# Optimization experiments

Measured on AMD Instinct MI355X. Metric: run time of the kernel, lower is better.

The kernel has to match this reference:

```python
import jax, jax.numpy as jnp
import numpy as np
from jax import lax


def _h0_entropy(img):
    """Persistence entropy of the 0-dim sublevel-set persistence diagram of a 2D
    image, using the vertex-based cubical complex (pixels = vertices, 4-neighbor
    edges with filtration value max(endpoints)). Essential (infinite) class is
    excluded. Computed via Kruskal-style union-find with the elder rule."""
    H, W = img.shape
    N = H * W
    vals = img.reshape(N)
    vals_sg = lax.stop_gradient(vals)  # pairing indices are non-differentiable

    idx = jnp.arange(N, dtype=jnp.int32).reshape(H, W)
    eu = jnp.concatenate([idx[:, :-1].ravel(), idx[:-1, :].ravel()])
    ev = jnp.concatenate([idx[:, 1:].ravel(), idx[1:, :].ravel()])
    E = eu.shape[0]  # H*(W-1) + (H-1)*W

    # process edges in increasing filtration order (sublevel filtration)
    w_sg = jnp.maximum(vals_sg[eu], vals_sg[ev])
    order = jnp.argsort(w_sg)
    eu = eu[order]
    ev = ev[order]

    def find(parent, u):
        return lax.while_loop(lambda x: parent[x] != x, lambda x: parent[x], u)

    def body(i, st):
        parent, rb, ob, odu, odv = st
        u = eu[i]
        v = ev[i]
        ru = find(parent, u)
        rv = find(parent, v)
        # one-shot path compression
        parent = parent.at[u].set(ru).at[v].set(rv)
        bu = rb[ru]  # birth-vertex index of each root's component
        bv = rb[rv]
        u_young = vals_sg[bu] >= vals_sg[bv]  # elder rule: later birth dies
        younger = jnp.where(u_young, ru, rv)
        elder = jnp.where(u_young, rv, ru)
        diff = ru != rv
        ob = ob.at[i].set(jnp.where(diff, rb[younger], -1))
        odu = odu.at[i].set(jnp.where(diff, u, 0))
        odv = odv.at[i].set(jnp.where(diff, v, 0))
        parent = parent.at[younger].set(jnp.where(diff, elder, younger))
        return (parent, rb, ob, odu, odv)

    init = (
        jnp.arange(N, dtype=jnp.int32),          # parent
        jnp.arange(N, dtype=jnp.int32),          # birth vertex per root
        -jnp.ones(E, dtype=jnp.int32),           # birth vertex per pair
        jnp.zeros(E, dtype=jnp.int32),           # death edge endpoint u
        jnp.zeros(E, dtype=jnp.int32),           # death edge endpoint v
    )
    _, _, ob, odu, odv = lax.fori_loop(0, E, body, init)

    valid = ob >= 0
    births = vals[jnp.clip(ob, 0)]
    deaths = jnp.maximum(vals[odu], vals[odv])
    pers = jnp.where(valid, deaths - births, 0.0)
    pers = jnp.maximum(pers, 0.0)
    total = jnp.sum(pers)
    p = pers / jnp.maximum(total, jnp.asarray(1e-12, pers.dtype))
    safe_p = jnp.where(p > 0, p, 1.0)
    return -jnp.sum(jnp.where(p > 0, p * jnp.log(safe_p), 0.0))


def setup_inputs() -> dict:
    key = jax.random.key(0)
    x = jax.random.normal(key, (8, 8, 96, 96), dtype=jnp.float32)
    return {"x": x}


def reference(x):
    B, C, H, W = x.shape
    flat = x.reshape(B * C, H, W)
    ents = jax.vmap(_h0_entropy)(flat)  # [B*C]
    # TopoHead stacks per-channel features along dim=1; maxdim=0 -> one
    # persistence-entropy value per (batch, channel).
    return ents.reshape(B, C, 1)
```

## Files before the change

### kernel.cpp

```cpp
#include <hip/hip_runtime.h>

#define H_ 96
#define W_ 96
#define NV (H_ * W_)
#define NT 1024
#define WELEM 576
#define NSUB 9

#define ARENA_BYTES 136192

__device__ __forceinline__ float keyToFloat(unsigned int k) {
  return __uint_as_float((k & 0x80000000u) ? (k ^ 0x80000000u) : ~k);
}
__device__ __forceinline__ unsigned int bitsToKey(unsigned int b) {
  return b ^ ((b & 0x80000000u) ? 0xFFFFFFFFu : 0x80000000u);
}

__global__ __launch_bounds__(NT, 1)
void topo_pk(const float* __restrict__ x, float* __restrict__ out) {
  __shared__ unsigned int arenaW[ARENA_BYTES / 4];
  __shared__ unsigned int waveS[16];
  __shared__ unsigned int waveB[16];
  __shared__ double Td[16], Sd[16];
  unsigned char* arena = (unsigned char*)arenaW;
  unsigned int*   Ka    = (unsigned int*)(arena);
  unsigned int*   Kb    = (unsigned int*)(arena + 36864);
  unsigned short* Pa    = (unsigned short*)(arena + 73728);
  unsigned short* Pb    = (unsigned short*)(arena + 92160);
  unsigned int*   hist  = (unsigned int*)(arena + 110592);
  unsigned char*  incB  = (unsigned char*)(arena + 126976);
  unsigned short* parU  = (unsigned short*)(arena + 92160);
  unsigned int*   claim = (unsigned int*)(arena + 36864);

  const int tid = threadIdx.x;
  const int wv = tid >> 6, ln = tid & 63;
  const float* img = x + (size_t)blockIdx.x * NV;

  const int wbase = wv * WELEM;
  for (int pass = 0; pass < 4; ++pass) {
    const unsigned int*   Ks = (pass & 1) ? Kb : Ka;
    const unsigned short* Ps = (pass & 1) ? Pb : Pa;
    unsigned int*   Kd = (pass & 1) ? Ka : Kb;
    unsigned short* Pd = (pass & 1) ? Pa : Pb;
    const int sh = pass << 3;

    for (int i = tid; i < 16 * 256; i += NT) hist[i] = 0u;
    __syncthreads();

    unsigned kreg[NSUB];
    unsigned rk[NSUB];
    #pragma unroll
    for (int j = 0; j < NSUB; ++j) {
      const int e = wbase + j * 64 + ln;
      const unsigned k = (pass == 0) ? bitsToKey(__float_as_uint(img[e])) : Ks[e];
      kreg[j] = k;
      const unsigned d = (k >> sh) & 255u;
      unsigned long long mask = ~0ull;
      #pragma unroll
      for (int b = 0; b < 8; ++b) {
        const unsigned long long bb = __ballot((d >> b) & 1u);
        mask &= ((d >> b) & 1u) ? bb : ~bb;
      }
      const unsigned long long below = mask & ((1ull << ln) - 1ull);
      const unsigned old = hist[wv * 256 + d];
      rk[j] = (d << 16) | (old + (unsigned)__popcll(below));
      if (below == 0ull)
        hist[wv * 256 + d] = old + (unsigned)__popcll(mask);
    }
    __syncthreads();

    {
      unsigned v0, v1, v2, v3;
      const int s0 = tid * 4;
      v0 = hist[((s0 + 0) & 15) * 256 + ((s0 + 0) >> 4)];
      v1 = hist[((s0 + 1) & 15) * 256 + ((s0 + 1) >> 4)];
      v2 = hist[((s0 + 2) & 15) * 256 + ((s0 + 2) >> 4)];
      v3 = hist[((s0 + 3) & 15) * 256 + ((s0 + 3) >> 4)];
      const unsigned ts = v0 + v1 + v2 + v3;
      unsigned incl = ts;
      #pragma unroll
      for (int off = 1; off < 64; off <<= 1) {
        const unsigned n = (unsigned)__shfl_up((int)incl, off, 64);
        if (ln >= off) incl += n;
      }
      if (ln == 63) waveS[wv] = incl;
      __syncthreads();
      if (tid < 16) {
        unsigned s = 0;
        for (int q = 0; q < 16; ++q) { if (q == tid) break; s += waveS[q]; }
        waveB[tid] = s;
      }
      __syncthreads();
      unsigned run = waveB[wv] + (incl - ts);
      hist[((s0 + 0) & 15) * 256 + ((s0 + 0) >> 4)] = run; run += v0;
      hist[((s0 + 1) & 15) * 256 + ((s0 + 1) >> 4)] = run; run += v1;
      hist[((s0 + 2) & 15) * 256 + ((s0 + 2) >> 4)] = run; run += v2;
      hist[((s0 + 3) & 15) * 256 + ((s0 + 3) >> 4)] = run;
    }
    __syncthreads();

    #pragma unroll
    for (int j = 0; j < NSUB; ++j) {
      const int e = wbase + j * 64 + ln;
      const unsigned d = rk[j] >> 16;
      const unsigned dest = hist[wv * 256 + d] + (rk[j] & 0xFFFFu);
      Kd[dest] = kreg[j];
      Pd[dest] = (pass == 0) ? (unsigned short)e : Ps[e];
    }
    __syncthreads();
  }

  for (int t = tid; t < NV; t += NT) parU[Pa[t]] = (unsigned short)(0x8000u | (unsigned)t);
  for (int i = tid; i < NV; i += NT) claim[i] = 0xFFFFFFFFu;
  for (int v = tid; v < NV; v += NT) {
    const unsigned kc = bitsToKey(__float_as_uint(img[v]));
    const int r = v / W_, c = v - r * W_;
    unsigned b = 0;
    if (c > 0       && bitsToKey(__float_as_uint(img[v - 1]))  <= kc) b |= 1u;
    if (c < W_ - 1  && bitsToKey(__float_as_uint(img[v + 1]))  <= kc) b |= 2u;
    if (r > 0       && bitsToKey(__float_as_uint(img[v - W_])) <= kc) b |= 4u;
    if (r < H_ - 1  && bitsToKey(__float_as_uint(img[v + W_])) <= kc) b |= 8u;
    incB[v] = (unsigned char)b;
  }
  __syncthreads();

  double T = 0.0, S = 0.0;
  unsigned gr = 0;
  for (int ch = 0; ch < NV / NT; ++ch) {
    const int t = ch * NT + tid;
    const int vid = (int)Pa[t];
    const float vt = keyToFloat(Ka[t]);
    const int nv0 = vid - 1, nv1 = vid + 1, nv2 = vid - W_, nv3 = vid + W_;
    const unsigned ib = incB[vid];
    const bool inc0 = (ib & 1u) != 0u;
    const bool inc1 = (ib & 2u) != 0u;
    const bool inc2 = (ib & 4u) != 0u;
    const bool inc3 = (ib & 8u) != 0u;
    int x0 = inc0 ? nv0 : vid, x1 = inc1 ? nv1 : vid;
    int x2 = inc2 ? nv2 : vid, x3 = inc3 ? nv3 : vid;
    unsigned e0 = 0, e1 = 0, e2 = 0, e3 = 0;
    bool committed = false;

    for (;;) {
      const unsigned cval = ((0x000FFFFFu - gr) << 10) | (unsigned)tid;
      ++gr;
      if (!committed) {
        bool d0 = !inc0, d1 = !inc1, d2 = !inc2, d3 = !inc3;
        while (!(d0 && d1 && d2 && d3)) {
          if (!d0) { unsigned e = parU[x0]; if (e & 0x8000u) { e0 = e; d0 = true; } else x0 = (int)e; }
          if (!d1) { unsigned e = parU[x1]; if (e & 0x8000u) { e1 = e; d1 = true; } else x1 = (int)e; }
          if (!d2) { unsigned e = parU[x2]; if (e & 0x8000u) { e2 = e; d2 = true; } else x2 = (int)e; }
          if (!d3) { unsigned e = parU[x3]; if (e & 0x8000u) { e3 = e; d3 = true; } else x3 = (int)e; }
        }
        if (inc0 && nv0 != x0) parU[nv0] = (unsigned short)x0;
        if (inc1 && nv1 != x1) parU[nv1] = (unsigned short)x1;
        if (inc2 && nv2 != x2) parU[nv2] = (unsigned short)x2;
        if (inc3 && nv3 != x3) parU[nv3] = (unsigned short)x3;
      }
      bool u0 = false, u1 = false, u2 = false, u3 = false, uv = false;
      int mvid = vid;
      int rr0 = 0, rr1 = 0, rr2 = 0, rr3 = 0;
      if (!committed) {
        int mrank = t;
        rr0 = (int)(e0 & 0x3FFFu); rr1 = (int)(e1 & 0x3FFFu);
        rr2 = (int)(e2 & 0x3FFFu); rr3 = (int)(e3 & 0x3FFFu);
        if (inc0 && rr0 < mrank) { mrank = rr0; mvid = x0; }
        if (inc1 && rr1 < mrank) { mrank = rr1; mvid = x1; }
        if (inc2 && rr2 < mrank) { mrank = rr2; mvid = x2; }
        if (inc3 && rr3 < mrank) { mrank = rr3; mvid = x3; }
        u0 = inc0 && (x0 != mvid);
        u1 = inc1 && (x1 != mvid) && !(inc0 && x1 == x0);
        u2 = inc2 && (x2 != mvid) && !(inc0 && x2 == x0) && !(inc1 && x2 == x1);
        u3 = inc3 && (x3 != mvid) && !(inc0 && x3 == x0) && !(inc1 && x3 == x1) && !(inc2 && x3 == x2);
        uv = (mvid != vid);
        if (u0) atomicMin(&claim[x0], cval);
        if (u1) atomicMin(&claim[x1], cval);
        if (u2) atomicMin(&claim[x2], cval);
        if (u3) atomicMin(&claim[x3], cval);
        if (uv) atomicMin(&claim[vid], cval);
      }
      __syncthreads();
      if (!committed) {
        bool win = true;
        if (u0 && claim[x0] != cval) win = false;
        if (u1 && claim[x1] != cval) win = false;
        if (u2 && claim[x2] != cval) win = false;
        if (u3 && claim[x3] != cval) win = false;
        if (uv && claim[vid] != cval) win = false;
        if (win) {
          if (u0) { const float p = vt - keyToFloat(Ka[rr0]);
                    if (p > 0.0f) { T += (double)p; S += (double)(p * logf(p)); }
                    parU[x0] = (unsigned short)mvid; }
          if (u1) { const float p = vt - keyToFloat(Ka[rr1]);
                    if (p > 0.0f) { T += (double)p; S += (double)(p * logf(p)); }
                    parU[x1] = (unsigned short)mvid; }
          if (u2) { const float p = vt - keyToFloat(Ka[rr2]);
                    if (p > 0.0f) { T += (double)p; S += (double)(p * logf(p)); }
                    parU[x2] = (unsigned short)mvid; }
          if (u3) { const float p = vt - keyToFloat(Ka[rr3]);
                    if (p > 0.0f) { T += (double)p; S += (double)(p * logf(p)); }
                    parU[x3] = (unsigned short)mvid; }
          if (uv) parU[vid] = (unsigned short)mvid;
          committed = true;
        }
      }
      if (__syncthreads_count(!committed ? 1 : 0) == 0) break;
    }
  }

  #pragma unroll
  for (int off = 32; off > 0; off >>= 1) {
    T += __shfl_down(T, off, 64);
    S += __shfl_down(S, off, 64);
  }
  if (ln == 0) { Td[wv] = T; Sd[wv] = S; }
  __syncthreads();
  if (tid == 0) {
    double Tt = 0.0, St = 0.0;
    for (int q = 0; q < 16; ++q) { Tt += Td[q]; St += Sd[q]; }
    out[blockIdx.x] = (Tt > 0.0) ? (float)(log(Tt) - St / Tt) : 0.0f;
  }
}

extern "C" void kernel_launch(void* const* d_in, const int* in_sizes, int n_in,
                              void* d_out, int out_size, void* d_ws, size_t ws_size,
                              hipStream_t stream) {
  (void)n_in; (void)out_size; (void)d_ws; (void)ws_size;
  const float* x = (const float*)d_in[0];
  float* out = (float*)d_out;
  int n_img = in_sizes[0] / NV;
  if (n_img <= 0) n_img = 1;
  topo_pk<<<n_img, NT, 0, stream>>>(x, out);
}
```

Before: 144.2 us.

## Split monolithic kernel into radix-sort and union-find kernels via workspace

The single per-image kernel is split into two launches. The first does the LDS radix sort and writes the sorted keys and permutation to the global workspace. The second reloads them and runs the parallel union-find and entropy reduction. Each kernel now uses less shared memory, which may change residency or scheduling, at the cost of an extra launch and a global round trip of about 55 KB per image. The old monolithic path is kept as a fallback when the workspace is too small.

```diff
diff --git a/kernel.cpp b/kernel.cpp
--- a/kernel.cpp
+++ b/kernel.cpp
@@ -7,7 +7,7 @@
 #define WELEM 576
 #define NSUB 9
 
-#define ARENA_BYTES 136192
+#define WS_STRIDE (64 * 1024)
 
 __device__ __forceinline__ float keyToFloat(unsigned int k) {
   return __uint_as_float((k & 0x80000000u) ? (k ^ 0x80000000u) : ~k);
@@ -17,24 +17,21 @@
 }
 
 __global__ __launch_bounds__(NT, 1)
-void topo_pk(const float* __restrict__ x, float* __restrict__ out) {
-  __shared__ unsigned int arenaW[ARENA_BYTES / 4];
+void kSort(const float* __restrict__ x, unsigned char* __restrict__ ws) {
+  __shared__ unsigned int arenaW[126976 / 4];
   __shared__ unsigned int waveS[16];
   __shared__ unsigned int waveB[16];
-  __shared__ double Td[16], Sd[16];
   unsigned char* arena = (unsigned char*)arenaW;
-  unsigned int*   Ka    = (unsigned int*)(arena);
-  unsigned int*   Kb    = (unsigned int*)(arena + 36864);
-  unsigned short* Pa    = (unsigned short*)(arena + 73728);
-  unsigned short* Pb    = (unsigned short*)(arena + 92160);
-  unsigned int*   hist  = (unsigned int*)(arena + 110592);
-  unsigned char*  incB  = (unsigned char*)(arena + 126976);
-  unsigned short* parU  = (unsigned short*)(arena + 92160);
-  unsigned int*   claim = (unsigned int*)(arena + 36864);
+  unsigned int*   Ka   = (unsigned int*)(arena);
+  unsigned int*   Kb   = (unsigned int*)(arena + 36864);
+  unsigned short* Pa   = (unsigned short*)(arena + 73728);
+  unsigned short* Pb   = (unsigned short*)(arena + 92160);
+  unsigned int*   hist = (unsigned int*)(arena + 110592);
 
   const int tid = threadIdx.x;
   const int wv = tid >> 6, ln = tid & 63;
   const float* img = x + (size_t)blockIdx.x * NV;
+  unsigned char* w = ws + (size_t)blockIdx.x * WS_STRIDE;
 
   const int wbase = wv * WELEM;
   for (int pass = 0; pass < 4; ++pass) {
@@ -109,6 +106,41 @@
     }
     __syncthreads();
   }
+
+  {
+    unsigned int* dK = (unsigned int*)(w);
+    for (int i = tid; i < NV; i += NT) dK[i] = Ka[i];
+    unsigned int* dP = (unsigned int*)(w + 36864);
+    const unsigned int* sP = (const unsigned int*)Pa;
+    for (int i = tid; i < NV / 2; i += NT) dP[i] = sP[i];
+  }
+}
+
+__global__ __launch_bounds__(NT, 1)
+void kUF(const float* __restrict__ x, const unsigned char* __restrict__ ws,
+         float* __restrict__ out) {
+  __shared__ unsigned int arenaW[119808 / 4];
+  __shared__ double Td[16], Sd[16];
+  unsigned char* arena = (unsigned char*)arenaW;
+  unsigned int*   Ka    = (unsigned int*)(arena);
+  unsigned short* Pa    = (unsigned short*)(arena + 36864);
+  unsigned short* parU  = (unsigned short*)(arena + 55296);
+  unsigned int*   claim = (unsigned int*)(arena + 73728);
+  unsigned char*  incB  = (unsigned char*)(arena + 110592);
+
+  const int tid = threadIdx.x;
+  const int wv = tid >> 6, ln = tid & 63;
+  const float* img = x + (size_t)blockIdx.x * NV;
+  const unsigned char* w = ws + (size_t)blockIdx.x * WS_STRIDE;
+
+  {
+    const unsigned int* sK = (const unsigned int*)(w);
+    for (int i = tid; i < NV; i += NT) Ka[i] = sK[i];
+    const unsigned int* sP = (const unsigned int*)(w + 36864);
+    unsigned int* dP = (unsigned int*)Pa;
+    for (int i = tid; i < NV / 2; i += NT) dP[i] = sP[i];
+  }
+  __syncthreads();
 
   for (int t = tid; t < NV; t += NT) parU[Pa[t]] = (unsigned short)(0x8000u | (unsigned)t);
   for (int i = tid; i < NV; i += NT) claim[i] = 0xFFFFFFFFu;
@@ -222,13 +254,217 @@
   }
 }
 
+__global__ __launch_bounds__(NT, 1)
+void topo_mono(const float* __restrict__ x, float* __restrict__ out) {
+  __shared__ unsigned int arenaW[136192 / 4];
+  __shared__ unsigned int waveS[16];
+  __shared__ unsigned int waveB[16];
+  __shared__ double Td[16], Sd[16];
+  unsigned char* arena = (unsigned char*)arenaW;
+  unsigned int*   Ka    = (unsigned int*)(arena);
+  unsigned int*   Kb    = (unsigned int*)(arena + 36864);
+  unsigned short* Pa    = (unsigned short*)(arena + 73728);
+  unsigned short* Pb    = (unsigned short*)(arena + 92160);
+  unsigned int*   hist  = (unsigned int*)(arena + 110592);
+  unsigned char*  incB  = (unsigned char*)(arena + 126976);
+  unsigned short* parU  = (unsigned short*)(arena + 92160);
+  unsigned int*   claim = (unsigned int*)(arena + 36864);
+
+  const int tid = threadIdx.x;
+  const int wv = tid >> 6, ln = tid & 63;
+  const float* img = x + (size_t)blockIdx.x * NV;
+
+  const int wbase = wv * WELEM;
+  for (int pass = 0; pass < 4; ++pass) {
+    const unsigned int*   Ks = (pass & 1) ? Kb : Ka;
+    const unsigned short* Ps = (pass & 1) ? Pb : Pa;
+    unsigned int*   Kd = (pass & 1) ? Ka : Kb;
+    unsigned short* Pd = (pass & 1) ? Pa : Pb;
+    const int sh = pass << 3;
+    for (int i = tid; i < 16 * 256; i += NT) hist[i] = 0u;
+    __syncthreads();
+    unsigned kreg[NSUB];
+    unsigned rk[NSUB];
+    #pragma unroll
+    for (int j = 0; j < NSUB; ++j) {
+      const int e = wbase + j * 64 + ln;
+      const unsigned k = (pass == 0) ? bitsToKey(__float_as_uint(img[e])) : Ks[e];
+      kreg[j] = k;
+      const unsigned d = (k >> sh) & 255u;
+      unsigned long long mask = ~0ull;
+      #pragma unroll
+      for (int b = 0; b < 8; ++b) {
+        const unsigned long long bb = __ballot((d >> b) & 1u);
+        mask &= ((d >> b) & 1u) ? bb : ~bb;
+      }
+      const unsigned long long below = mask & ((1ull << ln) - 1ull);
+      const unsigned old = hist[wv * 256 + d];
+      rk[j] = (d << 16) | (old + (unsigned)__popcll(below));
+      if (below == 0ull)
+        hist[wv * 256 + d] = old + (unsigned)__popcll(mask);
+    }
+    __syncthreads();
+    {
+      unsigned v0, v1, v2, v3;
+      const int s0 = tid * 4;
+      v0 = hist[((s0 + 0) & 15) * 256 + ((s0 + 0) >> 4)];
+      v1 = hist[((s0 + 1) & 15) * 256 + ((s0 + 1) >> 4)];
+      v2 = hist[((s0 + 2) & 15) * 256 + ((s0 + 2) >> 4)];
+      v3 = hist[((s0 + 3) & 15) * 256 + ((s0 + 3) >> 4)];
+      const unsigned ts = v0 + v1 + v2 + v3;
+      unsigned incl = ts;
+      #pragma unroll
+      for (int off = 1; off < 64; off <<= 1) {
+        const unsigned n = (unsigned)__shfl_up((int)incl, off, 64);
+        if (ln >= off) incl += n;
+      }
+      if (ln == 63) waveS[wv] = incl;
+      __syncthreads();
+      if (tid < 16) {
+        unsigned s = 0;
+        for (int q = 0; q < 16; ++q) { if (q == tid) break; s += waveS[q]; }
+        waveB[tid] = s;
+      }
+      __syncthreads();
+      unsigned run = waveB[wv] + (incl - ts);
+      hist[((s0 + 0) & 15) * 256 + ((s0 + 0) >> 4)] = run; run += v0;
+      hist[((s0 + 1) & 15) * 256 + ((s0 + 1) >> 4)] = run; run += v1;
+      hist[((s0 + 2) & 15) * 256 + ((s0 + 2) >> 4)] = run; run += v2;
+      hist[((s0 + 3) & 15) * 256 + ((s0 + 3) >> 4)] = run;
+    }
+    __syncthreads();
+    #pragma unroll
+    for (int j = 0; j < NSUB; ++j) {
+      const int e = wbase + j * 64 + ln;
+      const unsigned d = rk[j] >> 16;
+      const unsigned dest = hist[wv * 256 + d] + (rk[j] & 0xFFFFu);
+      Kd[dest] = kreg[j];
+      Pd[dest] = (pass == 0) ? (unsigned short)e : Ps[e];
+    }
+    __syncthreads();
+  }
+  for (int t = tid; t < NV; t += NT) parU[Pa[t]] = (unsigned short)(0x8000u | (unsigned)t);
+  for (int i = tid; i < NV; i += NT) claim[i] = 0xFFFFFFFFu;
+  for (int v = tid; v < NV; v += NT) {
+    const unsigned kc = bitsToKey(__float_as_uint(img[v]));
+    const int r = v / W_, c = v - r * W_;
+    unsigned b = 0;
+    if (c > 0       && bitsToKey(__float_as_uint(img[v - 1]))  <= kc) b |= 1u;
+    if (c < W_ - 1  && bitsToKey(__float_as_uint(img[v + 1]))  <= kc) b |= 2u;
+    if (r > 0       && bitsToKey(__float_as_uint(img[v - W_])) <= kc) b |= 4u;
+    if (r < H_ - 1  && bitsToKey(__float_as_uint(img[v + W_])) <= kc) b |= 8u;
+    incB[v] = (unsigned char)b;
+  }
+  __syncthreads();
+  double T = 0.0, S = 0.0;
+  unsigned gr = 0;
+  for (int ch = 0; ch < NV / NT; ++ch) {
+    const int t = ch * NT + tid;
+    const int vid = (int)Pa[t];
+    const float vt = keyToFloat(Ka[t]);
+    const int nv0 = vid - 1, nv1 = vid + 1, nv2 = vid - W_, nv3 = vid + W_;
+    const unsigned ib = incB[vid];
+    const bool inc0 = (ib & 1u) != 0u;
+    const bool inc1 = (ib & 2u) != 0u;
+    const bool inc2 = (ib & 4u) != 0u;
+    const bool inc3 = (ib & 8u) != 0u;
+    int x0 = inc0 ? nv0 : vid, x1 = inc1 ? nv1 : vid;
+    int x2 = inc2 ? nv2 : vid, x3 = inc3 ? nv3 : vid;
+    unsigned e0 = 0, e1 = 0, e2 = 0, e3 = 0;
+    bool committed = false;
+    for (;;) {
+      const unsigned cval = ((0x000FFFFFu - gr) << 10) | (unsigned)tid;
+      ++gr;
+      if (!committed) {
+        bool d0 = !inc0, d1 = !inc1, d2 = !inc2, d3 = !inc3;
+        while (!(d0 && d1 && d2 && d3)) {
+          if (!d0) { unsigned e = parU[x0]; if (e & 0x8000u) { e0 = e; d0 = true; } else x0 = (int)e; }
+          if (!d1) { unsigned e = parU[x1]; if (e & 0x8000u) { e1 = e; d1 = true; } else x1 = (int)e; }
+          if (!d2) { unsigned e = parU[x2]; if (e & 0x8000u) { e2 = e; d2 = true; } else x2 = (int)e; }
+          if (!d3) { unsigned e = parU[x3]; if (e & 0x8000u) { e3 = e; d3 = true; } else x3 = (int)e; }
+        }
+        if (inc0 && nv0 != x0) parU[nv0] = (unsigned short)x0;
+        if (inc1 && nv1 != x1) parU[nv1] = (unsigned short)x1;
+        if (inc2 && nv2 != x2) parU[nv2] = (unsigned short)x2;
+        if (inc3 && nv3 != x3) parU[nv3] = (unsigned short)x3;
+      }
+      bool u0 = false, u1 = false, u2 = false, u3 = false, uv = false;
+      int mvid = vid;
+      int rr0 = 0, rr1 = 0, rr2 = 0, rr3 = 0;
+      if (!committed) {
+        int mrank = t;
+        rr0 = (int)(e0 & 0x3FFFu); rr1 = (int)(e1 & 0x3FFFu);
+        rr2 = (int)(e2 & 0x3FFFu); rr3 = (int)(e3 & 0x3FFFu);
+        if (inc0 && rr0 < mrank) { mrank = rr0; mvid = x0; }
+        if (inc1 && rr1 < mrank) { mrank = rr1; mvid = x1; }
+        if (inc2 && rr2 < mrank) { mrank = rr2; mvid = x2; }
+        if (inc3 && rr3 < mrank) { mrank = rr3; mvid = x3; }
+        u0 = inc0 && (x0 != mvid);
+        u1 = inc1 && (x1 != mvid) && !(inc0 && x1 == x0);
+        u2 = inc2 && (x2 != mvid) && !(inc0 && x2 == x0) && !(inc1 && x2 == x1);
+        u3 = inc3 && (x3 != mvid) && !(inc0 && x3 == x0) && !(inc1 && x3 == x1) && !(inc2 && x3 == x2);
+        uv = (mvid != vid);
+        if (u0) atomicMin(&claim[x0], cval);
+        if (u1) atomicMin(&claim[x1], cval);
+        if (u2) atomicMin(&claim[x2], cval);
+        if (u3) atomicMin(&claim[x3], cval);
+        if (uv) atomicMin(&claim[vid], cval);
+      }
+      __syncthreads();
+      if (!committed) {
+        bool win = true;
+        if (u0 && claim[x0] != cval) win = false;
+        if (u1 && claim[x1] != cval) win = false;
+        if (u2 && claim[x2] != cval) win = false;
+        if (u3 && claim[x3] != cval) win = false;
+        if (uv && claim[vid] != cval) win = false;
+        if (win) {
+          if (u0) { const float p = vt - keyToFloat(Ka[rr0]);
+                    if (p > 0.0f) { T += (double)p; S += (double)(p * logf(p)); }
+                    parU[x0] = (unsigned short)mvid; }
+          if (u1) { const float p = vt - keyToFloat(Ka[rr1]);
+                    if (p > 0.0f) { T += (double)p; S += (double)(p * logf(p)); }
+                    parU[x1] = (unsigned short)mvid; }
+          if (u2) { const float p = vt - keyToFloat(Ka[rr2]);
+                    if (p > 0.0f) { T += (double)p; S += (double)(p * logf(p)); }
+                    parU[x2] = (unsigned short)mvid; }
+          if (u3) { const float p = vt - keyToFloat(Ka[rr3]);
+                    if (p > 0.0f) { T += (double)p; S += (double)(p * logf(p)); }
+                    parU[x3] = (unsigned short)mvid; }
+          if (uv) parU[vid] = (unsigned short)mvid;
+          committed = true;
+        }
+      }
+      if (__syncthreads_count(!committed ? 1 : 0) == 0) break;
+    }
+  }
+  #pragma unroll
+  for (int off = 32; off > 0; off >>= 1) {
+    T += __shfl_down(T, off, 64);
+    S += __shfl_down(S, off, 64);
+  }
+  if (ln == 0) { Td[wv] = T; Sd[wv] = S; }
+  __syncthreads();
+  if (tid == 0) {
+    double Tt = 0.0, St = 0.0;
+    for (int q = 0; q < 16; ++q) { Tt += Td[q]; St += Sd[q]; }
+    out[blockIdx.x] = (Tt > 0.0) ? (float)(log(Tt) - St / Tt) : 0.0f;
+  }
+}
+
 extern "C" void kernel_launch(void* const* d_in, const int* in_sizes, int n_in,
                               void* d_out, int out_size, void* d_ws, size_t ws_size,
                               hipStream_t stream) {
-  (void)n_in; (void)out_size; (void)d_ws; (void)ws_size;
+  (void)n_in; (void)out_size;
   const float* x = (const float*)d_in[0];
   float* out = (float*)d_out;
   int n_img = in_sizes[0] / NV;
   if (n_img <= 0) n_img = 1;
-  topo_pk<<<n_img, NT, 0, stream>>>(x, out);
-}
+  if (ws_size >= (size_t)n_img * WS_STRIDE) {
+    unsigned char* ws = (unsigned char*)d_ws;
+    kSort<<<n_img, NT, 0, stream>>>(x, ws);
+    kUF<<<n_img, NT, 0, stream>>>(x, ws, out);
+  } else {
+    topo_mono<<<n_img, NT, 0, stream>>>(x, out);
+  }
+}
```

Measured after the change: 147.4 us. +2.2%, slower.

## Process two sorted-vertex chunks per thread per claim round to halve barrier rounds

Applied to the files above, without the earlier changes.

Each thread now handles two vertices (from a 2048-wide window) per round of the claim/commit union-find loop instead of one, so the number of outer chunks drops from 9 to 5. This cuts the number of barrier-separated round sequences. The claim value now encodes the global vertex rank (14 bits) instead of the thread id, so conflicts between the two elements resolve by rank. The trade-off is wider windows, which may cause more claim conflicts and more retry rounds per window, plus more register pressure.

```diff
diff --git a/kernel.cpp b/kernel.cpp
--- a/kernel.cpp
+++ b/kernel.cpp
@@ -6,7 +6,6 @@
 #define NT 1024
 #define WELEM 576
 #define NSUB 9
-
 #define ARENA_BYTES 136192
 
 __device__ __forceinline__ float keyToFloat(unsigned int k) {
@@ -126,87 +125,156 @@
 
   double T = 0.0, S = 0.0;
   unsigned gr = 0;
-  for (int ch = 0; ch < NV / NT; ++ch) {
-    const int t = ch * NT + tid;
-    const int vid = (int)Pa[t];
-    const float vt = keyToFloat(Ka[t]);
-    const int nv0 = vid - 1, nv1 = vid + 1, nv2 = vid - W_, nv3 = vid + W_;
-    const unsigned ib = incB[vid];
-    const bool inc0 = (ib & 1u) != 0u;
-    const bool inc1 = (ib & 2u) != 0u;
-    const bool inc2 = (ib & 4u) != 0u;
-    const bool inc3 = (ib & 8u) != 0u;
-    int x0 = inc0 ? nv0 : vid, x1 = inc1 ? nv1 : vid;
-    int x2 = inc2 ? nv2 : vid, x3 = inc3 ? nv3 : vid;
-    unsigned e0 = 0, e1 = 0, e2 = 0, e3 = 0;
-    bool committed = false;
+
+  #define DECL_EV(Sfx) \
+    int vid##Sfx = 0, nv##Sfx##0 = 0, nv##Sfx##1 = 0, nv##Sfx##2 = 0, nv##Sfx##3 = 0; \
+    int x##Sfx##0 = 0, x##Sfx##1 = 0, x##Sfx##2 = 0, x##Sfx##3 = 0; \
+    unsigned e##Sfx##0 = 0, e##Sfx##1 = 0, e##Sfx##2 = 0, e##Sfx##3 = 0; \
+    bool in##Sfx##0 = false, in##Sfx##1 = false, in##Sfx##2 = false, in##Sfx##3 = false; \
+    float vt##Sfx = 0.f;
+
+  #define LOAD_EV(Sfx, tt) { \
+    vid##Sfx = (int)Pa[tt]; vt##Sfx = keyToFloat(Ka[tt]); \
+    const unsigned ib = incB[vid##Sfx]; \
+    nv##Sfx##0 = vid##Sfx - 1; nv##Sfx##1 = vid##Sfx + 1; \
+    nv##Sfx##2 = vid##Sfx - W_; nv##Sfx##3 = vid##Sfx + W_; \
+    in##Sfx##0 = (ib & 1u) != 0u; in##Sfx##1 = (ib & 2u) != 0u; \
+    in##Sfx##2 = (ib & 4u) != 0u; in##Sfx##3 = (ib & 8u) != 0u; \
+    x##Sfx##0 = in##Sfx##0 ? nv##Sfx##0 : vid##Sfx; \
+    x##Sfx##1 = in##Sfx##1 ? nv##Sfx##1 : vid##Sfx; \
+    x##Sfx##2 = in##Sfx##2 ? nv##Sfx##2 : vid##Sfx; \
+    x##Sfx##3 = in##Sfx##3 ? nv##Sfx##3 : vid##Sfx; \
+    e##Sfx##0 = e##Sfx##1 = e##Sfx##2 = e##Sfx##3 = 0; }
+
+  #define CHASE_COMPRESS(Sfx) { \
+    bool d0 = !in##Sfx##0, d1 = !in##Sfx##1, d2 = !in##Sfx##2, d3 = !in##Sfx##3; \
+    while (!(d0 && d1 && d2 && d3)) { \
+      if (!d0) { unsigned e = parU[x##Sfx##0]; if (e & 0x8000u) { e##Sfx##0 = e; d0 = true; } else x##Sfx##0 = (int)e; } \
+      if (!d1) { unsigned e = parU[x##Sfx##1]; if (e & 0x8000u) { e##Sfx##1 = e; d1 = true; } else x##Sfx##1 = (int)e; } \
+      if (!d2) { unsigned e = parU[x##Sfx##2]; if (e & 0x8000u) { e##Sfx##2 = e; d2 = true; } else x##Sfx##2 = (int)e; } \
+      if (!d3) { unsigned e = parU[x##Sfx##3]; if (e & 0x8000u) { e##Sfx##3 = e; d3 = true; } else x##Sfx##3 = (int)e; } \
+    } \
+    if (in##Sfx##0 && nv##Sfx##0 != x##Sfx##0) parU[nv##Sfx##0] = (unsigned short)x##Sfx##0; \
+    if (in##Sfx##1 && nv##Sfx##1 != x##Sfx##1) parU[nv##Sfx##1] = (unsigned short)x##Sfx##1; \
+    if (in##Sfx##2 && nv##Sfx##2 != x##Sfx##2) parU[nv##Sfx##2] = (unsigned short)x##Sfx##2; \
+    if (in##Sfx##3 && nv##Sfx##3 != x##Sfx##3) parU[nv##Sfx##3] = (unsigned short)x##Sfx##3; }
+
+  for (int w = 0; w < 5; ++w) {
+    const int base2 = w * 2048;
+    const int tA = base2 + tid;
+    const int tB = base2 + NT + tid;
+    DECL_EV(A)
+    DECL_EV(B)
+    bool cmA = false, cmB = (tB >= NV);
+    LOAD_EV(A, tA)
+    if (!cmB) LOAD_EV(B, tB)
 
     for (;;) {
-      const unsigned cval = ((0x000FFFFFu - gr) << 10) | (unsigned)tid;
+      const unsigned ep = (0x3FFFFu - gr) << 14;
       ++gr;
-      if (!committed) {
-        bool d0 = !inc0, d1 = !inc1, d2 = !inc2, d3 = !inc3;
-        while (!(d0 && d1 && d2 && d3)) {
-          if (!d0) { unsigned e = parU[x0]; if (e & 0x8000u) { e0 = e; d0 = true; } else x0 = (int)e; }
-          if (!d1) { unsigned e = parU[x1]; if (e & 0x8000u) { e1 = e; d1 = true; } else x1 = (int)e; }
-          if (!d2) { unsigned e = parU[x2]; if (e & 0x8000u) { e2 = e; d2 = true; } else x2 = (int)e; }
-          if (!d3) { unsigned e = parU[x3]; if (e & 0x8000u) { e3 = e; d3 = true; } else x3 = (int)e; }
+      const unsigned cvalA = ep | (unsigned)tA;
+      const unsigned cvalB = ep | (unsigned)tB;
+      bool uA0 = false, uA1 = false, uA2 = false, uA3 = false, uvA = false;
+      bool uB0 = false, uB1 = false, uB2 = false, uB3 = false, uvB = false;
+      int mvidA = 0, mvidB = 0;
+      int rA0 = 0, rA1 = 0, rA2 = 0, rA3 = 0;
+      int rB0 = 0, rB1 = 0, rB2 = 0, rB3 = 0;
+
+      if (!cmA) {
+        CHASE_COMPRESS(A)
+        int mrank = tA; mvidA = vidA;
+        rA0 = (int)(eA0 & 0x3FFFu); rA1 = (int)(eA1 & 0x3FFFu);
+        rA2 = (int)(eA2 & 0x3FFFu); rA3 = (int)(eA3 & 0x3FFFu);
+        if (inA0 && rA0 < mrank) { mrank = rA0; mvidA = xA0; }
+        if (inA1 && rA1 < mrank) { mrank = rA1; mvidA = xA1; }
+        if (inA2 && rA2 < mrank) { mrank = rA2; mvidA = xA2; }
+        if (inA3 && rA3 < mrank) { mrank = rA3; mvidA = xA3; }
+        uA0 = inA0 && (xA0 != mvidA);
+        uA1 = inA1 && (xA1 != mvidA) && !(inA0 && xA1 == xA0);
+        uA2 = inA2 && (xA2 != mvidA) && !(inA0 && xA2 == xA0) && !(inA1 && xA2 == xA1);
+        uA3 = inA3 && (xA3 != mvidA) && !(inA0 && xA3 == xA0) && !(inA1 && xA3 == xA1) && !(inA2 && xA3 == xA2);
+        uvA = (mvidA != vidA);
+        if (uA0) atomicMin(&claim[xA0], cvalA);
+        if (uA1) atomicMin(&claim[xA1], cvalA);
+        if (uA2) atomicMin(&claim[xA2], cvalA);
+        if (uA3) atomicMin(&claim[xA3], cvalA);
+        if (uvA) atomicMin(&claim[vidA], cvalA);
+      }
+      if (!cmB) {
+        CHASE_COMPRESS(B)
+        int mrank = tB; mvidB = vidB;
+        rB0 = (int)(eB0 & 0x3FFFu); rB1 = (int)(eB1 & 0x3FFFu);
+        rB2 = (int)(eB2 & 0x3FFFu); rB3 = (int)(eB3 & 0x3FFFu);
+        if (inB0 && rB0 < mrank) { mrank = rB0; mvidB = xB0; }
+        if (inB1 && rB1 < mrank) { mrank = rB1; mvidB = xB1; }
+        if (inB2 && rB2 < mrank) { mrank = rB2; mvidB = xB2; }
+        if (inB3 && rB3 < mrank) { mrank = rB3; mvidB = xB3; }
+        uB0 = inB0 && (xB0 != mvidB);
+        uB1 = inB1 && (xB1 != mvidB) && !(inB0 && xB1 == xB0);
+        uB2 = inB2 && (xB2 != mvidB) && !(inB0 && xB2 == xB0) && !(inB1 && xB2 == xB1);
+        uB3 = inB3 && (xB3 != mvidB) && !(inB0 && xB3 == xB0) && !(inB1 && xB3 == xB1) && !(inB2 && xB3 == xB2);
+        uvB = (mvidB != vidB);
+        if (uB0) atomicMin(&claim[xB0], cvalB);
+        if (uB1) atomicMin(&claim[xB1], cvalB);
+        if (uB2) atomicMin(&claim[xB2], cvalB);
+        if (uB3) atomicMin(&claim[xB3], cvalB);
+        if (uvB) atomicMin(&claim[vidB], cvalB);
+      }
+      __syncthreads();
+      if (!cmA) {
+        bool win = true;
+        if (uA0 && claim[xA0] != cvalA) win = false;
+        if (uA1 && claim[xA1] != cvalA) win = false;
+        if (uA2 && claim[xA2] != cvalA) win = false;
+        if (uA3 && claim[xA3] != cvalA) win = false;
+        if (uvA && claim[vidA] != cvalA) win = false;
+        if (win) {
+          if (uA0) { const float p = vtA - keyToFloat(Ka[rA0]);
+                     if (p > 0.0f) { T += (double)p; S += (double)(p * logf(p)); }
+                     parU[xA0] = (unsigned short)mvidA; }
+          if (uA1) { const float p = vtA - keyToFloat(Ka[rA1]);
+                     if (p > 0.0f) { T += (double)p; S += (double)(p * logf(p)); }
+                     parU[xA1] = (unsigned short)mvidA; }
+          if (uA2) { const float p = vtA - keyToFloat(Ka[rA2]);
+                     if (p > 0.0f) { T += (double)p; S += (double)(p * logf(p)); }
+                     parU[xA2] = (unsigned short)mvidA; }
+          if (uA3) { const float p = vtA - keyToFloat(Ka[rA3]);
+                     if (p > 0.0f) { T += (double)p; S += (double)(p * logf(p)); }
+                     parU[xA3] = (unsigned short)mvidA; }
+          if (uvA) parU[vidA] = (unsigned short)mvidA;
+          cmA = true;
         }
-        if (inc0 && nv0 != x0) parU[nv0] = (unsigned short)x0;
-        if (inc1 && nv1 != x1) parU[nv1] = (unsigned short)x1;
-        if (inc2 && nv2 != x2) parU[nv2] = (unsigned short)x2;
-        if (inc3 && nv3 != x3) parU[nv3] = (unsigned short)x3;
-      }
-      bool u0 = false, u1 = false, u2 = false, u3 = false, uv = false;
-      int mvid = vid;
-      int rr0 = 0, rr1 = 0, rr2 = 0, rr3 = 0;
-      if (!committed) {
-        int mrank = t;
-        rr0 = (int)(e0 & 0x3FFFu); rr1 = (int)(e1 & 0x3FFFu);
-        rr2 = (int)(e2 & 0x3FFFu); rr3 = (int)(e3 & 0x3FFFu);
-        if (inc0 && rr0 < mrank) { mrank = rr0; mvid = x0; }
-        if (inc1 && rr1 < mrank) { mrank = rr1; mvid = x1; }
-        if (inc2 && rr2 < mrank) { mrank = rr2; mvid = x2; }
-        if (inc3 && rr3 < mrank) { mrank = rr3; mvid = x3; }
-        u0 = inc0 && (x0 != mvid);
-        u1 = inc1 && (x1 != mvid) && !(inc0 && x1 == x0);
-        u2 = inc2 && (x2 != mvid) && !(inc0 && x2 == x0) && !(inc1 && x2 == x1);
-        u3 = inc3 && (x3 != mvid) && !(inc0 && x3 == x0) && !(inc1 && x3 == x1) && !(inc2 && x3 == x2);
-        uv = (mvid != vid);
-        if (u0) atomicMin(&claim[x0], cval);
-        if (u1) atomicMin(&claim[x1], cval);
-        if (u2) atomicMin(&claim[x2], cval);
-        if (u3) atomicMin(&claim[x3], cval);
-        if (uv) atomicMin(&claim[vid], cval);
-      }
-      __syncthreads();
-      if (!committed) {
+      }
+      if (!cmB) {
         bool win = true;
-        if (u0 && claim[x0] != cval) win = false;
-        if (u1 && claim[x1] != cval) win = false;
-        if (u2 && claim[x2] != cval) win = false;
-        if (u3 && claim[x3] != cval) win = false;
-        if (uv && claim[vid] != cval) win = false;
+        if (uB0 && claim[xB0] != cvalB) win = false;
+        if (uB1 && claim[xB1] != cvalB) win = false;
+        if (uB2 && claim[xB2] != cvalB) win = false;
+        if (uB3 && claim[xB3] != cvalB) win = false;
+        if (uvB && claim[vidB] != cvalB) win = false;
         if (win) {
-          if (u0) { const float p = vt - keyToFloat(Ka[rr0]);
-                    if (p > 0.0f) { T += (double)p; S += (double)(p * logf(p)); }
-                    parU[x0] = (unsigned short)mvid; }
-          if (u1) { const float p = vt - keyToFloat(Ka[rr1]);
-                    if (p > 0.0f) { T += (double)p; S += (double)(p * logf(p)); }
-                    parU[x1] = (unsigned short)mvid; }
-          if (u2) { const float p = vt - keyToFloat(Ka[rr2]);
-                    if (p > 0.0f) { T += (double)p; S += (double)(p * logf(p)); }
-                    parU[x2] = (unsigned short)mvid; }
-          if (u3) { const float p = vt - keyToFloat(Ka[rr3]);
-                    if (p > 0.0f) { T += (double)p; S += (double)(p * logf(p)); }
-                    parU[x3] = (unsigned short)mvid; }
-          if (uv) parU[vid] = (unsigned short)mvid;
-          committed = true;
+          if (uB0) { const float p = vtB - keyToFloat(Ka[rB0]);
+                     if (p > 0.0f) { T += (double)p; S += (double)(p * logf(p)); }
+                     parU[xB0] = (unsigned short)mvidB; }
+          if (uB1) { const float p = vtB - keyToFloat(Ka[rB1]);
+                     if (p > 0.0f) { T += (double)p; S += (double)(p * logf(p)); }
+                     parU[xB1] = (unsigned short)mvidB; }
+          if (uB2) { const float p = vtB - keyToFloat(Ka[rB2]);
+                     if (p > 0.0f) { T += (double)p; S += (double)(p * logf(p)); }
+                     parU[xB2] = (unsigned short)mvidB; }
+          if (uB3) { const float p = vtB - keyToFloat(Ka[rB3]);
+                     if (p > 0.0f) { T += (double)p; S += (double)(p * logf(p)); }
+                     parU[xB3] = (unsigned short)mvidB; }
+          if (uvB) parU[vidB] = (unsigned short)mvidB;
+          cmB = true;
         }
       }
-      if (__syncthreads_count(!committed ? 1 : 0) == 0) break;
+      if (__syncthreads_count((cmA ? 0 : 1) + (cmB ? 0 : 1)) == 0) break;
     }
   }
+  #undef DECL_EV
+  #undef LOAD_EV
+  #undef CHASE_COMPRESS
 
   #pragma unroll
   for (int off = 32; off > 0; off >>= 1) {
```

Measured after the change: 151.2 us. 1.05x slower.
